# Optimization experiments

Measured on AMD Instinct MI355X. Metric: run time of the kernel, lower is better.

The kernel has to match this reference:

```python
import jax, jax.numpy as jnp
import numpy as np

NUM_HEADS = 8

B, N, M = 2, 10000, 320000
QD = KD = HD = 256


def setup_inputs() -> dict:
    key = jax.random.key(0)
    k1, k2, k3, k4, k5 = jax.random.split(key, 5)
    x_q = jax.random.normal(k1, (B, N, QD), dtype=jnp.float32)
    x_k = jax.random.normal(k2, (B, N, KD), dtype=jnp.float32)
    mask = jax.random.randint(k3, (2, M), 0, N, dtype=jnp.int64)
    # xavier_uniform: limit = sqrt(6/(fan_in+fan_out))
    lim_q = float(np.sqrt(6.0 / (QD + HD)))
    lim_k = float(np.sqrt(6.0 / (KD + HD)))
    w_q = jax.random.uniform(k4, (QD, HD), minval=-lim_q, maxval=lim_q, dtype=jnp.float32)
    w_k = jax.random.uniform(k5, (KD, HD), minval=-lim_k, maxval=lim_k, dtype=jnp.float32)
    return {"x_q": x_q, "x_k": x_k, "mask": mask, "w_q": w_q, "w_k": w_k}


def reference(x_q, x_k, mask, w_q, w_k):
    b, n, _ = x_q.shape
    m = mask.shape[1]
    d = w_q.shape[1]          # hidden_dim
    h = NUM_HEADS
    dh = d // h
    q = x_q @ w_q             # (b, n, d)
    k = x_k @ w_k             # (b, n, d)
    # edge gather + elementwise multiply
    prod = q[:, mask[0], :] * k[:, mask[1], :]            # (b, m, d)
    # head buffer is i // (d/h): contiguous blocks -> reshape-sum
    a = prod.reshape(b, m, h, dh).sum(axis=-1)            # (b, m, h)
    a = a / jnp.sqrt(jnp.float32(w_k.shape[0]))           # / sqrt(key_dim)
    # segment softmax over destination index = mask[1 - reduce_dim], reduce_dim=1 -> mask[0]
    idx = mask[0]
    a = a - a.max()                                       # global max, as in source
    e = jnp.exp(a)                                        # (b, m, h)
    seg = jnp.zeros((b, n, h), e.dtype).at[:, idx, :].add(e)
    return e / (seg[:, idx, :] + 1e-16)
```

## Files before the change

kernel.cpp:

```cpp
#include <hip/hip_runtime.h>
#include <hip/hip_bf16.h>
#include <hip/hip_fp16.h>

#define DHID 256
#define NHEAD 8
#define BATCH 2

typedef _Float16 h8 __attribute__((ext_vector_type(8)));
typedef float f4 __attribute__((ext_vector_type(4)));

__global__ __launch_bounds__(256) void prep_kernel(
    const float* __restrict__ Wq, const float* __restrict__ Wk,
    _Float16* __restrict__ Wtq, _Float16* __restrict__ Wtk,
    float* __restrict__ seg, int segN)
{
    if (blockIdx.z == 2) {
        int idx = (blockIdx.x * 8 + blockIdx.y) * 256 + threadIdx.y * 32 + threadIdx.x;
        for (int i = idx; i < segN; i += 64 * 256) seg[i] = 0.f;
        return;
    }
    const float* W = blockIdx.z ? Wk : Wq;
    _Float16* Wt   = blockIdx.z ? Wtk : Wtq;
    __shared__ float tile[32][33];
    const int tx = threadIdx.x;
    const int ty = threadIdx.y;
    const int n0 = blockIdx.x * 32;
    const int k0 = blockIdx.y * 32;
#pragma unroll
    for (int j = 0; j < 32; j += 8)
        tile[ty + j][tx] = W[(size_t)(k0 + ty + j) * DHID + n0 + tx];
    __syncthreads();
#pragma unroll
    for (int j = 0; j < 32; j += 8)
        Wt[(size_t)(n0 + ty + j) * DHID + k0 + tx] = (_Float16)tile[tx][ty + j];
}

__global__ __launch_bounds__(256, 2) void gemm_mfma(
    const float* __restrict__ Xq, const float* __restrict__ Xk,
    const _Float16* __restrict__ Wtq, const _Float16* __restrict__ Wtk,
    _Float16* __restrict__ Qh, _Float16* __restrict__ Kh, int Mrows)
{
    __shared__ _Float16 As[64 * 256];
    __shared__ _Float16 Bs[64 * 256];

    const int t    = threadIdx.x;
    const int lane = t & 63;
    const int wave = t >> 6;
    const int rowBase = blockIdx.x * 64;
    const int ar   = wave * 16 + (lane & 15);
    const int quad = lane >> 4;

    for (int z = 0; z < 2; ++z) {
        const float* X     = z ? Xk : Xq;
        const _Float16* Wt = z ? Wtk : Wtq;
        _Float16* C        = z ? Kh : Qh;

#pragma unroll
        for (int i = 0; i < 8; ++i) {
            int idx = t + i * 256;
            int row = idx >> 5;
            int c   = idx & 31;
            int grow = rowBase + row;
            f4 v0 = {0,0,0,0}, v1 = {0,0,0,0};
            if (grow < Mrows) {
                const float* p = X + (size_t)grow * DHID + c * 8;
                v0 = *(const f4*)p;
                v1 = *(const f4*)(p + 4);
            }
            h8 hv;
            hv[0]=(_Float16)v0[0]; hv[1]=(_Float16)v0[1]; hv[2]=(_Float16)v0[2]; hv[3]=(_Float16)v0[3];
            hv[4]=(_Float16)v1[0]; hv[5]=(_Float16)v1[1]; hv[6]=(_Float16)v1[2]; hv[7]=(_Float16)v1[3];
            int sc = c ^ (row & 7);
            *(h8*)&As[row * 256 + sc * 8] = hv;
        }

        for (int ct64 = 0; ct64 < 4; ++ct64) {
#pragma unroll
            for (int i = 0; i < 8; ++i) {
                int idx = t + i * 256;
                int n = idx >> 5;
                int c = idx & 31;
                h8 hv = *(const h8*)(Wt + (size_t)(ct64 * 64 + n) * DHID + c * 8);
                int sc = c ^ (n & 7);
                *(h8*)&Bs[n * 256 + sc * 8] = hv;
            }
            __syncthreads();

            f4 acc[4] = {{0,0,0,0},{0,0,0,0},{0,0,0,0},{0,0,0,0}};
#pragma unroll
            for (int kc = 0; kc < 8; ++kc) {
                int ac = (kc * 4 + quad) ^ (ar & 7);
                h8 afrag = *(const h8*)&As[ar * 256 + ac * 8];
#pragma unroll
                for (int ct = 0; ct < 4; ++ct) {
                    int bn = ct * 16 + (lane & 15);
                    int bc = (kc * 4 + quad) ^ (bn & 7);
                    h8 bfrag = *(const h8*)&Bs[bn * 256 + bc * 8];
                    acc[ct] = __builtin_amdgcn_mfma_f32_16x16x32_f16(afrag, bfrag, acc[ct], 0, 0, 0);
                }
            }

#pragma unroll
            for (int ct = 0; ct < 4; ++ct) {
#pragma unroll
                for (int r = 0; r < 4; ++r) {
                    int grow = rowBase + wave * 16 + quad * 4 + r;
                    if (grow < Mrows)
                        C[(size_t)grow * DHID + ct64 * 64 + ct * 16 + (lane & 15)] = (_Float16)acc[ct][r];
                }
            }
            __syncthreads();
        }
    }
}

__global__ __launch_bounds__(256, 6) void edge_kernel(
    const _Float16* __restrict__ Qh, const _Float16* __restrict__ Kh,
    const int* __restrict__ mask, _Float16* __restrict__ eh,
    float* __restrict__ seg, int M, int N)
{
    const int lane = threadIdx.x & 63;
    const int wave = threadIdx.x >> 6;
    const int c    = lane & 31;
    const int half = lane >> 5;
    const int h    = c >> 2;
    const long e0 = ((long)blockIdx.x * 4 + wave) * 8;
    const int b = blockIdx.y;
    if (e0 >= M) return;

    int idxv = 0;
    {
        long le = e0 + (lane & 7);
        if (le >= M) le = M - 1;
        if (lane < 8)       idxv = mask[le];
        else if (lane < 16) idxv = mask[M + le];
    }

    const _Float16* Qb = Qh + (size_t)b * N * DHID;
    const _Float16* Kb = Kh + (size_t)b * N * DHID;

    int sidx[4], didx[4];
#pragma unroll
    for (int p = 0; p < 4; ++p) {
        sidx[p] = __shfl(idxv, p * 2 + half);
        didx[p] = __shfl(idxv, 8 + p * 2 + half);
    }

    h8 qv[4], kv[4];
#pragma unroll
    for (int p = 0; p < 4; ++p) {
        qv[p] = *(const h8*)(Qb + (size_t)sidx[p] * DHID + c * 8);
        kv[p] = *(const h8*)(Kb + (size_t)didx[p] * DHID + c * 8);
    }

#pragma unroll
    for (int p = 0; p < 4; ++p) {
        float s = 0.f;
#pragma unroll
        for (int u = 0; u < 8; ++u)
            s += (float)qv[p][u] * (float)kv[p][u];
        s += __shfl_xor(s, 1);
        s += __shfl_xor(s, 2);
        const long e = e0 + p * 2 + half;
        if ((c & 3) == 0 && e < M) {
            _Float16 evh = (_Float16)expf(s * 0.0625f);
            __builtin_nontemporal_store(evh, &eh[((size_t)b * M + e) * NHEAD + h]);
            atomicAdd(seg + ((size_t)b * N + sidx[p]) * NHEAD + h, (float)evh);
        }
    }
}

__global__ __launch_bounds__(256) void norm_kernel(
    const int* __restrict__ mask, const float* __restrict__ seg,
    const _Float16* __restrict__ eh, float* __restrict__ out,
    int M, int N, int BM)
{
    int idx = blockIdx.x * 256 + threadIdx.x;
    if (idx >= BM) return;
    int b = idx / M;
    int e = idx - b * M;
    int src = mask[e];
    const f4* s4 = (const f4*)(seg + ((size_t)b * N + src) * NHEAD);
    f4 s0 = s4[0], s1 = s4[1];
    h8 ev = *(const h8*)(eh + (size_t)idx * NHEAD);
    f4 o0, o1;
    o0[0] = (float)ev[0] * __builtin_amdgcn_rcpf(s0[0] + 1e-16f);
    o0[1] = (float)ev[1] * __builtin_amdgcn_rcpf(s0[1] + 1e-16f);
    o0[2] = (float)ev[2] * __builtin_amdgcn_rcpf(s0[2] + 1e-16f);
    o0[3] = (float)ev[3] * __builtin_amdgcn_rcpf(s0[3] + 1e-16f);
    o1[0] = (float)ev[4] * __builtin_amdgcn_rcpf(s1[0] + 1e-16f);
    o1[1] = (float)ev[5] * __builtin_amdgcn_rcpf(s1[1] + 1e-16f);
    o1[2] = (float)ev[6] * __builtin_amdgcn_rcpf(s1[2] + 1e-16f);
    o1[3] = (float)ev[7] * __builtin_amdgcn_rcpf(s1[3] + 1e-16f);
    f4* o4 = (f4*)(out + (size_t)idx * NHEAD);
    __builtin_nontemporal_store(o0, &o4[0]);
    __builtin_nontemporal_store(o1, &o4[1]);
}

extern "C" void kernel_launch(void* const* d_in, const int* in_sizes, int n_in,
                              void* d_out, int out_size, void* d_ws, size_t ws_size,
                              hipStream_t stream) {
    const float* x_q  = (const float*)d_in[0];
    const float* x_k  = (const float*)d_in[1];
    const int*   mask = (const int*)d_in[2];
    const float* w_q  = (const float*)d_in[3];
    const float* w_k  = (const float*)d_in[4];
    float* out = (float*)d_out;

    const int M = in_sizes[2] / 2;
    const int N = in_sizes[0] / (BATCH * DHID);
    const int Mrows = BATCH * N;

    _Float16* Qh  = (_Float16*)d_ws;
    _Float16* Kh  = Qh  + (size_t)Mrows * DHID;
    _Float16* Wtq = Kh  + (size_t)Mrows * DHID;
    _Float16* Wtk = Wtq + (size_t)DHID * DHID;
    float*    seg = (float*)(Wtk + (size_t)DHID * DHID);
    _Float16* eh  = (_Float16*)(seg + (size_t)BATCH * N * NHEAD);

    prep_kernel<<<dim3(DHID / 32, DHID / 32, 3), dim3(32, 8), 0, stream>>>(
        w_q, w_k, Wtq, Wtk, seg, BATCH * N * NHEAD);

    gemm_mfma<<<dim3((Mrows + 63) / 64), 256, 0, stream>>>(
        x_q, x_k, Wtq, Wtk, Qh, Kh, Mrows);

    long waves = (M + 7) / 8;
    dim3 egrid((unsigned)((waves + 3) / 4), BATCH);
    edge_kernel<<<egrid, 256, 0, stream>>>(Qh, Kh, mask, eh, seg, M, N);

    const int BM = BATCH * M;
    norm_kernel<<<(BM + 255) / 256, 256, 0, stream>>>(mask, seg, eh, out, M, N, BM);
}
```

Measured before the change: 184.2 us.

## Split Q/K GEMM across grid z and move seg zeroing into GEMM

The GEMM kernel now runs the Q and K projections as separate blocks along grid z instead of looping over both inside one block. This doubles the block count (about 313 to 626) to fill more CUs. The seg buffer zeroing moves from the weight-prep kernel into 8 extra GEMM blocks with vectorized stores, shortening prep. The cost is that each block loads its own As tile, which it already did per z before, so there is little duplication.

```diff
diff --git a/kernel.cpp b/kernel.cpp
--- a/kernel.cpp
+++ b/kernel.cpp
@@ -11,14 +11,8 @@
 
 __global__ __launch_bounds__(256) void prep_kernel(
     const float* __restrict__ Wq, const float* __restrict__ Wk,
-    _Float16* __restrict__ Wtq, _Float16* __restrict__ Wtk,
-    float* __restrict__ seg, int segN)
-{
-    if (blockIdx.z == 2) {
-        int idx = (blockIdx.x * 8 + blockIdx.y) * 256 + threadIdx.y * 32 + threadIdx.x;
-        for (int i = idx; i < segN; i += 64 * 256) seg[i] = 0.f;
-        return;
-    }
+    _Float16* __restrict__ Wtq, _Float16* __restrict__ Wtk)
+{
     const float* W = blockIdx.z ? Wk : Wq;
     _Float16* Wt   = blockIdx.z ? Wtk : Wtq;
     __shared__ float tile[32][33];
@@ -38,79 +32,89 @@
 __global__ __launch_bounds__(256, 2) void gemm_mfma(
     const float* __restrict__ Xq, const float* __restrict__ Xk,
     const _Float16* __restrict__ Wtq, const _Float16* __restrict__ Wtk,
-    _Float16* __restrict__ Qh, _Float16* __restrict__ Kh, int Mrows)
-{
+    _Float16* __restrict__ Qh, _Float16* __restrict__ Kh,
+    float* __restrict__ seg, int segN, int nx, int Mrows)
+{
+    const int t = threadIdx.x;
+    if ((int)blockIdx.x >= nx) {
+        if (blockIdx.z == 0) {
+            int base = ((int)blockIdx.x - nx) * 256 + t;
+            f4 z = {0.f, 0.f, 0.f, 0.f};
+            for (int i = base; i < segN / 4; i += 8 * 256)
+                ((f4*)seg)[i] = z;
+        }
+        return;
+    }
+
+    const float* X       = blockIdx.z ? Xk : Xq;
+    const _Float16* Wt   = blockIdx.z ? Wtk : Wtq;
+    _Float16* C          = blockIdx.z ? Kh : Qh;
+
     __shared__ _Float16 As[64 * 256];
     __shared__ _Float16 Bs[64 * 256];
 
-    const int t    = threadIdx.x;
     const int lane = t & 63;
     const int wave = t >> 6;
     const int rowBase = blockIdx.x * 64;
+
+#pragma unroll
+    for (int i = 0; i < 8; ++i) {
+        int idx = t + i * 256;
+        int row = idx >> 5;
+        int c   = idx & 31;
+        int grow = rowBase + row;
+        f4 v0 = {0,0,0,0}, v1 = {0,0,0,0};
+        if (grow < Mrows) {
+            const float* p = X + (size_t)grow * DHID + c * 8;
+            v0 = *(const f4*)p;
+            v1 = *(const f4*)(p + 4);
+        }
+        h8 hv;
+        hv[0]=(_Float16)v0[0]; hv[1]=(_Float16)v0[1]; hv[2]=(_Float16)v0[2]; hv[3]=(_Float16)v0[3];
+        hv[4]=(_Float16)v1[0]; hv[5]=(_Float16)v1[1]; hv[6]=(_Float16)v1[2]; hv[7]=(_Float16)v1[3];
+        int sc = c ^ (row & 7);
+        *(h8*)&As[row * 256 + sc * 8] = hv;
+    }
+
     const int ar   = wave * 16 + (lane & 15);
     const int quad = lane >> 4;
 
-    for (int z = 0; z < 2; ++z) {
-        const float* X     = z ? Xk : Xq;
-        const _Float16* Wt = z ? Wtk : Wtq;
-        _Float16* C        = z ? Kh : Qh;
-
+    for (int ct64 = 0; ct64 < 4; ++ct64) {
 #pragma unroll
         for (int i = 0; i < 8; ++i) {
             int idx = t + i * 256;
-            int row = idx >> 5;
-            int c   = idx & 31;
-            int grow = rowBase + row;
-            f4 v0 = {0,0,0,0}, v1 = {0,0,0,0};
-            if (grow < Mrows) {
-                const float* p = X + (size_t)grow * DHID + c * 8;
-                v0 = *(const f4*)p;
-                v1 = *(const f4*)(p + 4);
+            int n = idx >> 5;
+            int c = idx & 31;
+            h8 hv = *(const h8*)(Wt + (size_t)(ct64 * 64 + n) * DHID + c * 8);
+            int sc = c ^ (n & 7);
+            *(h8*)&Bs[n * 256 + sc * 8] = hv;
+        }
+        __syncthreads();
+
+        f4 acc[4] = {{0,0,0,0},{0,0,0,0},{0,0,0,0},{0,0,0,0}};
+#pragma unroll
+        for (int kc = 0; kc < 8; ++kc) {
+            int ac = (kc * 4 + quad) ^ (ar & 7);
+            h8 afrag = *(const h8*)&As[ar * 256 + ac * 8];
+#pragma unroll
+            for (int ct = 0; ct < 4; ++ct) {
+                int bn = ct * 16 + (lane & 15);
+                int bc = (kc * 4 + quad) ^ (bn & 7);
+                h8 bfrag = *(const h8*)&Bs[bn * 256 + bc * 8];
+                acc[ct] = __builtin_amdgcn_mfma_f32_16x16x32_f16(afrag, bfrag, acc[ct], 0, 0, 0);
             }
-            h8 hv;
-            hv[0]=(_Float16)v0[0]; hv[1]=(_Float16)v0[1]; hv[2]=(_Float16)v0[2]; hv[3]=(_Float16)v0[3];
-            hv[4]=(_Float16)v1[0]; hv[5]=(_Float16)v1[1]; hv[6]=(_Float16)v1[2]; hv[7]=(_Float16)v1[3];
-            int sc = c ^ (row & 7);
-            *(h8*)&As[row * 256 + sc * 8] = hv;
-        }
-
-        for (int ct64 = 0; ct64 < 4; ++ct64) {
-#pragma unroll
-            for (int i = 0; i < 8; ++i) {
-                int idx = t + i * 256;
-                int n = idx >> 5;
-                int c = idx & 31;
-                h8 hv = *(const h8*)(Wt + (size_t)(ct64 * 64 + n) * DHID + c * 8);
-                int sc = c ^ (n & 7);
-                *(h8*)&Bs[n * 256 + sc * 8] = hv;
+        }
+
+#pragma unroll
+        for (int ct = 0; ct < 4; ++ct) {
+#pragma unroll
+            for (int r = 0; r < 4; ++r) {
+                int grow = rowBase + wave * 16 + quad * 4 + r;
+                if (grow < Mrows)
+                    C[(size_t)grow * DHID + ct64 * 64 + ct * 16 + (lane & 15)] = (_Float16)acc[ct][r];
             }
-            __syncthreads();
-
-            f4 acc[4] = {{0,0,0,0},{0,0,0,0},{0,0,0,0},{0,0,0,0}};
-#pragma unroll
-            for (int kc = 0; kc < 8; ++kc) {
-                int ac = (kc * 4 + quad) ^ (ar & 7);
-                h8 afrag = *(const h8*)&As[ar * 256 + ac * 8];
-#pragma unroll
-                for (int ct = 0; ct < 4; ++ct) {
-                    int bn = ct * 16 + (lane & 15);
-                    int bc = (kc * 4 + quad) ^ (bn & 7);
-                    h8 bfrag = *(const h8*)&Bs[bn * 256 + bc * 8];
-                    acc[ct] = __builtin_amdgcn_mfma_f32_16x16x32_f16(afrag, bfrag, acc[ct], 0, 0, 0);
-                }
-            }
-
-#pragma unroll
-            for (int ct = 0; ct < 4; ++ct) {
-#pragma unroll
-                for (int r = 0; r < 4; ++r) {
-                    int grow = rowBase + wave * 16 + quad * 4 + r;
-                    if (grow < Mrows)
-                        C[(size_t)grow * DHID + ct64 * 64 + ct * 16 + (lane & 15)] = (_Float16)acc[ct][r];
-                }
-            }
-            __syncthreads();
-        }
+        }
+        __syncthreads();
     }
 }
 
@@ -210,19 +214,21 @@
     const int M = in_sizes[2] / 2;
     const int N = in_sizes[0] / (BATCH * DHID);
     const int Mrows = BATCH * N;
+    const int segN  = BATCH * N * NHEAD;
 
     _Float16* Qh  = (_Float16*)d_ws;
     _Float16* Kh  = Qh  + (size_t)Mrows * DHID;
     _Float16* Wtq = Kh  + (size_t)Mrows * DHID;
     _Float16* Wtk = Wtq + (size_t)DHID * DHID;
     float*    seg = (float*)(Wtk + (size_t)DHID * DHID);
-    _Float16* eh  = (_Float16*)(seg + (size_t)BATCH * N * NHEAD);
-
-    prep_kernel<<<dim3(DHID / 32, DHID / 32, 3), dim3(32, 8), 0, stream>>>(
-        w_q, w_k, Wtq, Wtk, seg, BATCH * N * NHEAD);
-
-    gemm_mfma<<<dim3((Mrows + 63) / 64), 256, 0, stream>>>(
-        x_q, x_k, Wtq, Wtk, Qh, Kh, Mrows);
+    _Float16* eh  = (_Float16*)(seg + (size_t)segN);
+
+    prep_kernel<<<dim3(DHID / 32, DHID / 32, 2), dim3(32, 8), 0, stream>>>(
+        w_q, w_k, Wtq, Wtk);
+
+    const int nx = (Mrows + 63) / 64;
+    gemm_mfma<<<dim3(nx + 8, 1, 2), 256, 0, stream>>>(
+        x_q, x_k, Wtq, Wtk, Qh, Kh, seg, segN, nx, Mrows);
 
     long waves = (M + 7) / 8;
     dim3 egrid((unsigned)((waves + 3) / 4), BATCH);
```

Measured after the change: 181.4 us. About the same (-1.5%).
